# Optimization experiments

Hardware: AMD Instinct MI355X
Metric: run time of the kernel (lower is better)

The kernel has to match this reference:

```python
import jax, jax.numpy as jnp
import numpy as np

NQ = 7
DIM = 2 ** NQ  # 128
N_LAYERS = 3

# Pauli-Z sign tables over the 128 basis states (wire 0 = most significant bit)
_bits = ((np.arange(DIM)[None, :] >> (NQ - 1 - np.arange(NQ)[:, None])) & 1)
_SZ = (1.0 - 2.0 * _bits).astype(np.float32)            # [7, 128]
_SZZ = (_SZ * np.roll(_SZ, -1, axis=0)).astype(np.float32)  # [7, 128], Z_i Z_{(i+1)%7}


def _cnot_perm(c, t):
    # CNOT is a basis-state permutation: flip target bit where control bit = 1
    k = np.arange(DIM)
    return k ^ (((k >> (NQ - 1 - c)) & 1) << (NQ - 1 - t))


def _apply_ry(state, theta, q):
    # state: [B, 128] complex64; theta: [B] or scalar (real)
    B = state.shape[0]
    s = state.reshape(B, 2 ** q, 2, 2 ** (NQ - 1 - q))
    c = jnp.reshape(jnp.cos(0.5 * theta), (-1, 1, 1))
    sn = jnp.reshape(jnp.sin(0.5 * theta), (-1, 1, 1))
    a0, a1 = s[:, :, 0, :], s[:, :, 1, :]
    return jnp.stack([c * a0 - sn * a1, sn * a0 + c * a1], axis=2).reshape(B, DIM)


def _apply_rz(state, theta, q):
    B = state.shape[0]
    s = state.reshape(B, 2 ** q, 2, 2 ** (NQ - 1 - q))
    p = jnp.reshape(jnp.exp(-0.5j * theta), (-1, 1, 1))  # diag(e^{-i t/2}, e^{+i t/2})
    return jnp.stack([p * s[:, :, 0, :], jnp.conj(p) * s[:, :, 1, :]], axis=2).reshape(B, DIM)


def _circuit(x_q, scales, biases, wry, wrz):
    # Batched 7-qubit state-vector simulation of quantum_circuit_v3
    B = x_q.shape[0]
    state = jnp.zeros((B, DIM), jnp.complex64).at[:, 0].set(1.0)
    ang = scales[None, :] * x_q + biases[None, :]  # [B, 7] encoding angles (same every layer)
    for layer in range(N_LAYERS):
        for i in range(NQ):
            state = _apply_ry(state, ang[:, i], i)
        for i in range(NQ):
            state = _apply_ry(state, wry[layer, i], i)
            state = _apply_rz(state, wrz[layer, i], i)
        shift = layer + 1
        for i in range(NQ):
            state = state[:, _cnot_perm(i, (i + shift) % NQ)]
    probs = state.real ** 2 + state.imag ** 2  # [B, 128]
    return jnp.concatenate([probs @ _SZ.T, probs @ _SZZ.T], axis=1)  # [B, 14]


def setup_inputs() -> dict:
    key = jax.random.key(0)
    ks = jax.random.split(key, 16)
    B, F = 32768, 64
    fus_in = 14 + 32 + F  # 110
    lin = lambda k, fi, fo: (0.05 * jax.random.normal(k, (fi, fo), jnp.float32))
    d = {
        "x_q": jax.random.uniform(ks[0], (B, NQ), jnp.float32),
        "x_c": jax.random.normal(ks[1], (B, F), jnp.float32),
        "input_scales": jnp.full((NQ,), np.pi, jnp.float32),
        "input_biases": jnp.zeros((NQ,), jnp.float32),
        "q_params_ry": 0.1 * jax.random.normal(ks[2], (N_LAYERS, NQ), jnp.float32),
        "q_params_rz": 0.1 * jax.random.normal(ks[3], (N_LAYERS, NQ), jnp.float32),
        "enc_w1": lin(ks[4], F, 64), "enc_b1": jnp.zeros((64,), jnp.float32),
        "enc_w2": lin(ks[5], 64, 32), "enc_b2": jnp.zeros((32,), jnp.float32),
        "fus_w1": lin(ks[6], fus_in, 128), "fus_b1": jnp.zeros((128,), jnp.float32),
        "fus_w2": lin(ks[7], 128, 64), "fus_b2": jnp.zeros((64,), jnp.float32),
        "fus_w3": lin(ks[8], 64, 32), "fus_b3": jnp.zeros((32,), jnp.float32),
        "fus_w4": lin(ks[9], 32, 1), "fus_b4": jnp.zeros((1,), jnp.float32),
    }
    return d


def reference(x_q, x_c, input_scales, input_biases, q_params_ry, q_params_rz,
              enc_w1, enc_b1, enc_w2, enc_b2,
              fus_w1, fus_b1, fus_w2, fus_b2, fus_w3, fus_b3, fus_w4, fus_b4):
    q_out = _circuit(x_q, input_scales, input_biases, q_params_ry, q_params_rz)  # [B, 14]
    h = jax.nn.relu(x_c @ enc_w1 + enc_b1)
    c_enc = jax.nn.relu(h @ enc_w2 + enc_b2)  # [B, 32]
    comb = jnp.concatenate([q_out, c_enc, x_c], axis=1)  # [B, 110]
    h = jax.nn.relu(comb @ fus_w1 + fus_b1)
    h = jax.nn.relu(h @ fus_w2 + fus_b2)
    h = jax.nn.relu(h @ fus_w3 + fus_b3)
    return (h @ fus_w4 + fus_b4)[:, 0]  # [B], dropout is identity at inference
```

## Files before the change

kernel.cpp:

```cpp
#include <hip/hip_runtime.h>
#include <math.h>

#define NQ 7
#define DIM 128
#define NLAYERS 3
#define ROWS 64
#define LDS_S 136

typedef __attribute__((ext_vector_type(8))) short bf16x8;
typedef __attribute__((ext_vector_type(4))) float f32x4;
typedef __attribute__((ext_vector_type(2))) float f32x2;
typedef __attribute__((ext_vector_type(4))) unsigned short us4;

__device__ __forceinline__ unsigned short f2bf(float x) {
    union { float f; unsigned int u; } v; v.f = x;
    unsigned int r = v.u + 0x7fff + ((v.u >> 16) & 1);
    return (unsigned short)(r >> 16);
}
__device__ __forceinline__ f32x2 sp(float x) { return (f32x2){x, x}; }
__device__ __forceinline__ f32x2 sel2(int c, f32x2 a, f32x2 b) {
    f32x2 r; r.x = c ? a.x : b.x; r.y = c ? a.y : b.y; return r;
}

constexpr int cperm(int k, int c, int t) {
    return k ^ (((k >> (6 - c)) & 1) << (6 - t));
}
constexpr int lgather(int k, int s) {
    int r = k;
    for (int i = 6; i >= 0; --i) r = cperm(r, i, (i + s) % 7);
    return r;
}

struct Mat { int c[7]; };

constexpr Mat ID{{1, 2, 4, 8, 16, 32, 64}};

constexpr int parity7(int x) { x ^= x >> 4; x ^= x >> 2; x ^= x >> 1; return x & 1; }

constexpr int mapv(const Mat& A, int v) {
    int r = 0;
    for (int j = 0; j < 7; ++j) if ((v >> j) & 1) r ^= A.c[j];
    return r;
}
constexpr Mat matmul(const Mat& A, const Mat& B) {
    Mat m{};
    for (int j = 0; j < 7; ++j) m.c[j] = mapv(A, B.c[j]);
    return m;
}
constexpr Mat matG(int L) {
    Mat m{};
    for (int j = 0; j < 7; ++j) m.c[j] = lgather(1 << j, L + 1);
    return m;
}
constexpr Mat matinv(const Mat& A) {
    int M[7] = {};
    for (int r = 0; r < 7; ++r) {
        int row = 0;
        for (int j = 0; j < 7; ++j) row |= ((A.c[j] >> r) & 1) << j;
        M[r] = row | (1 << (7 + r));
    }
    for (int col = 0; col < 7; ++col) {
        int piv = col;
        while (!((M[piv] >> col) & 1)) ++piv;
        int t = M[col]; M[col] = M[piv]; M[piv] = t;
        for (int r = 0; r < 7; ++r)
            if (r != col && ((M[r] >> col) & 1)) M[r] ^= M[col];
    }
    Mat inv{};
    for (int j = 0; j < 7; ++j) {
        int c = 0;
        for (int r = 0; r < 7; ++r) c |= ((M[r] >> (7 + j)) & 1) << r;
        inv.c[j] = c;
    }
    return inv;
}
constexpr bool isident(const Mat& A) {
    for (int j = 0; j < 7; ++j) if (A.c[j] != (1 << j)) return false;
    return true;
}

constexpr Mat LAM1  = matinv(matG(0));
constexpr Mat LAM2  = matmul(matinv(matG(1)), LAM1);
constexpr Mat LAM3  = matmul(matinv(matG(2)), LAM2);
constexpr Mat LAM1I = matG(0);
constexpr Mat LAM2I = matinv(LAM2);
static_assert(isident(matmul(LAM1, LAM1I)), "lam1 inv");
static_assert(isident(matmul(LAM2, LAM2I)), "lam2 inv");
static_assert(isident(matmul(matG(2), matmul(LAM3, matinv(LAM2)))), "lam3 chain");

constexpr int rowmask(const Mat& A, int b) {
    int r = 0;
    for (int j = 0; j < 7; ++j) r |= ((A.c[j] >> b) & 1) << j;
    return r;
}
constexpr int featM(const Mat& A, int m) {
    int M = 0;
    for (int j = 0; j < 7; ++j) M |= parity7(A.c[j] & m) << j;
    return M;
}
constexpr int szzmask(int i) { return (1 << (6 - i)) | (1 << (6 - ((i + 1) % 7))); }
constexpr int kmask(int k) { return (k < 7) ? (64 >> k) : szzmask(k - 7); }
constexpr unsigned pack_feat(int base) {
    unsigned r = 0;
    for (int j = 0; j < 4; ++j) {
        int k = base + j;
        unsigned e = (k < 14) ? (unsigned)featM(LAM3, kmask(k)) : 0u;
        r |= e << (8 * j);
    }
    return r;
}

template<int M>
__device__ __forceinline__ float xsh(float v) {
    if constexpr (M == 1 || M == 2 || M == 3) {
        constexpr int ctrl = (0 ^ M) | ((1 ^ M) << 2) | ((2 ^ M) << 4) | ((3 ^ M) << 6);
        return __int_as_float(__builtin_amdgcn_update_dpp(
            __float_as_int(v), __float_as_int(v), ctrl, 0xF, 0xF, true));
    } else if constexpr (M == 7) {
        return __int_as_float(__builtin_amdgcn_update_dpp(
            __float_as_int(v), __float_as_int(v), 0x141, 0xF, 0xF, true));
    } else if constexpr (M == 8) {
        return __int_as_float(__builtin_amdgcn_update_dpp(
            __float_as_int(v), __float_as_int(v), 0x128, 0xF, 0xF, true));
    } else if constexpr (M == 15) {
        return __int_as_float(__builtin_amdgcn_update_dpp(
            __float_as_int(v), __float_as_int(v), 0x140, 0xF, 0xF, true));
    } else if constexpr (M < 32) {
        return __int_as_float(__builtin_amdgcn_ds_swizzle(
            __float_as_int(v), (M << 10) | 0x1F));
    } else {
        return __shfl_xor(v, M, 64);
    }
}
template<int M>
__device__ __forceinline__ f32x2 xsh2(f32x2 v) {
    f32x2 r; r.x = xsh<M>(v.x); r.y = xsh<M>(v.y); return r;
}

__device__ __forceinline__ float bpermf(int addr, float v) {
    return __int_as_float(__builtin_amdgcn_ds_bpermute(addr, __float_as_int(v)));
}

template<int D, int R>
__device__ __forceinline__ void ryg(f32x2 c, f32x2 s, int lane,
                                    f32x2& x0r, f32x2& x0i, f32x2& x1r, f32x2& x1i)
{
    constexpr int  DL = D & 63;
    constexpr int  RL = R & 63;
    constexpr bool D6 = (D >> 6) & 1;
    constexpr bool R6 = (R >> 6) & 1;
    int par = __popc(lane & RL) & 1;
    f32x2 ns  = -s;
    f32x2 sg0 = sel2(par, s, ns);
    f32x2 sg1 = R6 ? sel2(par, ns, s) : sg0;
    f32x2 p0r, p0i, p1r, p1i;
    if constexpr (D6) {
        if constexpr (DL == 0) { p0r = x1r; p0i = x1i; p1r = x0r; p1i = x0i; }
        else {
            p0r = xsh2<DL>(x1r); p0i = xsh2<DL>(x1i);
            p1r = xsh2<DL>(x0r); p1i = xsh2<DL>(x0i);
        }
    } else {
        p0r = xsh2<DL>(x0r); p0i = xsh2<DL>(x0i);
        p1r = xsh2<DL>(x1r); p1i = xsh2<DL>(x1i);
    }
    x0r = c * x0r + sg0 * p0r;  x0i = c * x0i + sg0 * p0i;
    x1r = c * x1r + sg1 * p1r;  x1i = c * x1i + sg1 * p1i;
}

template<int LYR, int I>
__device__ __forceinline__ void rygates(
    const float* trig, const f32x2 (&dc)[NQ], const f32x2 (&dsn)[NQ], int lane,
    f32x2& A0r, f32x2& A0i, f32x2& A1r, f32x2& A1i)
{
    if constexpr (I < NQ) {
        constexpr Mat LM  = (LYR == 1) ? LAM1 : LAM2;
        constexpr Mat LMI = (LYR == 1) ? LAM1I : LAM2I;
        constexpr int b   = 6 - I;
        constexpr int D   = mapv(LMI, 1 << b);
        constexpr int R   = rowmask(LM, b);
        float cw = trig[(LYR * NQ + I) * 2 + 0];
        float sw = trig[(LYR * NQ + I) * 2 + 1];
        f32x2 c = dc[I] * sp(cw) - dsn[I] * sp(sw);
        f32x2 s = dsn[I] * sp(cw) + dc[I] * sp(sw);
        ryg<D, R>(c, s, lane, A0r, A0i, A1r, A1i);
        rygates<LYR, I + 1>(trig, dc, dsn, lane, A0r, A0i, A1r, A1i);
    }
}

template<int LYR, int Q>
__device__ __forceinline__ void rzrows(const float* __restrict__ wrz, int lane,
                                       float& Aacc, float& Bacc)
{
    if constexpr (Q < NQ) {
        constexpr Mat LM = (LYR == 0) ? ID : ((LYR == 1) ? LAM1 : LAM2);
        constexpr int R  = rowmask(LM, 6 - Q);
        float h = 0.5f * wrz[LYR * NQ + Q];
        float t = (__popc(lane & (R & 63)) & 1) ? -h : h;
        if constexpr ((R >> 6) & 1) Bacc += t; else Aacc += t;
        rzrows<LYR, Q + 1>(wrz, lane, Aacc, Bacc);
    }
}

template<int LYR>
__device__ __forceinline__ void rzlayer(const float* __restrict__ wrz, int lane,
    f32x2& A0r, f32x2& A0i, f32x2& A1r, f32x2& A1i)
{
    float Aacc = 0.0f, Bacc = 0.0f;
    rzrows<LYR, 0>(wrz, lane, Aacc, Bacc);
    float th0 = Aacc + Bacc, th1 = Aacc - Bacc;
    float c0 = __cosf(th0), s0 = __sinf(th0);
    float c1 = __cosf(th1), s1 = __sinf(th1);
    f32x2 r, im;
    r = A0r; im = A0i;
    A0r = sp(c0) * r  + sp(s0) * im;
    A0i = sp(c0) * im - sp(s0) * r;
    r = A1r; im = A1i;
    A1r = sp(c1) * r  + sp(s1) * im;
    A1i = sp(c1) * im - sp(s1) * r;
}

template<int M>
__device__ __forceinline__ void bfly2(int lane, f32x2& tp, f32x2& tm) {
    f32x2 pp = xsh2<M>(tp), pm = xsh2<M>(tm);
    int hi = lane & M;
    tp = sel2(hi, pp - tp, tp + pp);
    tm = sel2(hi, pm - tm, tm + pm);
}

__global__ __launch_bounds__(256) void circuit_kernel(
    const float* __restrict__ x_q, const float* __restrict__ scales,
    const float* __restrict__ biases,
    const float* __restrict__ wry, const float* __restrict__ wrz,
    const float* __restrict__ ew1, const float* __restrict__ ew2,
    const float* __restrict__ w1,  const float* __restrict__ w2,
    const float* __restrict__ w3,  const float* __restrict__ w4,
    float* __restrict__ q_out,
    unsigned short* __restrict__ ew1t, unsigned short* __restrict__ ew2t,
    unsigned short* __restrict__ w1t,  unsigned short* __restrict__ w2t,
    unsigned short* __restrict__ w3t,  unsigned short* __restrict__ w4t,
    int B)
{
    __shared__ float strig[NLAYERS * NQ * 2];
    const int tid  = threadIdx.x;
    const int lane = tid & 63;

    if (tid < NLAYERS * NQ) {
        float hy = 0.5f * wry[tid];
        strig[tid * 2 + 0] = __cosf(hy);
        strig[tid * 2 + 1] = __sinf(hy);
    }

    if (blockIdx.x < 64) {
        const int gbase  = blockIdx.x * 256 + tid;
        const int stride = 64 * 256;
        for (int i = gbase; i < 16384; i += stride) {
            int n = i >> 7, kp = i & 127;
            unsigned short v = 0;
            if (kp < 64)        v = f2bf(w1[(46 + kp) * 128 + n]);
            else if (kp < 78)   v = f2bf(w1[(kp - 64) * 128 + n]);
            else if (kp < 110)  v = f2bf(w1[(kp - 78 + 14) * 128 + n]);
            w1t[i] = v;
        }
        for (int i = gbase; i < 8192; i += stride) {
            int n = i >> 7, k = i & 127;
            w2t[i] = f2bf(w2[k * 64 + n]);
        }
        for (int i = gbase; i < 4096; i += stride) {
            int n = i >> 6, k = i & 63;
            ew1t[i] = f2bf(ew1[k * 64 + n]);
        }
        for (int i = gbase; i < 2048; i += stride) {
            int n = i >> 6, k = i & 63;
            ew2t[i] = f2bf(ew2[k * 32 + n]);
        }
        for (int i = gbase; i < 2048; i += stride) {
            int n = i >> 6, k = i & 63;
            w3t[i] = f2bf(w3[k * 32 + n]);
        }
        for (int i = gbase; i < 512; i += stride) {
            int n = i >> 5, k = i & 31;
            w4t[i] = (n == 0) ? f2bf(w4[k]) : (unsigned short)0;
        }
    }
    __syncthreads();

    int gtid = blockIdx.x * blockDim.x + tid;
    int wv   = gtid >> 6;
    int e0   = wv * 2;
    if (e0 >= B) return;

    f32x2 dc[NQ], dsn[NQ];
#pragma unroll
    for (int i = 0; i < NQ; ++i) {
        float h0 = 0.5f * fmaf(scales[i], x_q[(size_t)e0 * NQ + i], biases[i]);
        float h1 = 0.5f * fmaf(scales[i], x_q[(size_t)(e0 + 1) * NQ + i], biases[i]);
        dc[i]  = (f32x2){__cosf(h0), __cosf(h1)};
        dsn[i] = (f32x2){__sinf(h0), __sinf(h1)};
    }

    f32x2 A0r, A0i = sp(0.0f), A1r, A1i = sp(0.0f);
    {
        f32x2 cl[NQ], sl[NQ];
#pragma unroll
        for (int i = 0; i < NQ; ++i) {
            float cw = strig[i * 2 + 0], sw = strig[i * 2 + 1];
            cl[i] = dc[i] * sp(cw) - dsn[i] * sp(sw);
            sl[i] = dsn[i] * sp(cw) + dc[i] * sp(sw);
        }
        f32x2 f1 = sel2(lane & 32, sl[1], cl[1]);
        f32x2 f2 = sel2(lane & 16, sl[2], cl[2]);
        f32x2 f3 = sel2(lane &  8, sl[3], cl[3]);
        f32x2 f4 = sel2(lane &  4, sl[4], cl[4]);
        f32x2 f5 = sel2(lane &  2, sl[5], cl[5]);
        f32x2 f6 = sel2(lane &  1, sl[6], cl[6]);
        f32x2 pr = (f1 * f2) * (f3 * f4) * (f5 * f6);
        A0r = pr * cl[0];
        A1r = pr * sl[0];
    }

    rzlayer<0>(wrz, lane, A0r, A0i, A1r, A1i);
    rygates<1, 0>(strig, dc, dsn, lane, A0r, A0i, A1r, A1i);
    rzlayer<1>(wrz, lane, A0r, A0i, A1r, A1i);
    rygates<2, 0>(strig, dc, dsn, lane, A0r, A0i, A1r, A1i);
    rzlayer<2>(wrz, lane, A0r, A0i, A1r, A1i);

    f32x2 p0 = A0r * A0r + A0i * A0i;
    f32x2 p1 = A1r * A1r + A1i * A1i;
    f32x2 tp = p0 + p1;
    f32x2 tm = p0 - p1;

    bfly2<1>(lane, tp, tm);
    bfly2<2>(lane, tp, tm);
    bfly2<4>(lane, tp, tm);
    bfly2<8>(lane, tp, tm);
    bfly2<16>(lane, tp, tm);
    bfly2<32>(lane, tp, tm);

    {
        constexpr unsigned P0 = pack_feat(0),  P1 = pack_feat(4);
        constexpr unsigned P2 = pack_feat(8),  P3 = pack_feat(12);
        int k = lane & 15;
        unsigned wlo  = (k & 4) ? P1 : P0;
        unsigned whi  = (k & 4) ? P3 : P2;
        unsigned word = (k & 8) ? whi : wlo;
        unsigned entry = (word >> ((k & 3) * 8)) & 127u;
        int addr   = (int)(entry & 63u) << 2;
        int useTm  = (int)(entry & 64u);
        int e      = (lane >> 4) & 1;
        float vpx = bpermf(addr, tp.x), vpy = bpermf(addr, tp.y);
        float vmx = bpermf(addr, tm.x), vmy = bpermf(addr, tm.y);
        float vp = e ? vpy : vpx;
        float vm = e ? vmy : vmx;
        float val = useTm ? vm : vp;
        if (lane < 32) q_out[(size_t)e0 * 16 + lane] = val;
    }
}

template<int K, int NT, bool RELU>
__device__ __forceinline__ void wlayer(
    const unsigned short* src, unsigned short* dst,
    const unsigned short* __restrict__ wt, const float* __restrict__ bias,
    int dstcol, int lane)
{
    constexpr int KB = K / 32;
    const int lcol = lane & 15;
    const int lrow = lane >> 4;

    bf16x8 a[KB];
#pragma unroll
    for (int kb = 0; kb < KB; ++kb)
        a[kb] = *(const bf16x8*)&src[lcol * LDS_S + kb * 32 + lrow * 8];

#pragma unroll
    for (int n = 0; n < NT; ++n) {
        float bb = bias[n * 16 + lcol];
        f32x4 acc = (f32x4){bb, bb, bb, bb};
#pragma unroll
        for (int kb = 0; kb < KB; ++kb) {
            bf16x8 b = *(const bf16x8*)&wt[(n * 16 + lcol) * K + kb * 32 + lrow * 8];
            acc = __builtin_amdgcn_mfma_f32_16x16x32_bf16(a[kb], b, acc, 0, 0, 0);
        }
#pragma unroll
        for (int r = 0; r < 4; ++r) {
            float v = acc[r];
            if (RELU) v = fmaxf(v, 0.0f);
            dst[(lrow * 4 + r) * LDS_S + dstcol + n * 16 + lcol] = f2bf(v);
        }
    }
}

__global__ __launch_bounds__(256) void mlp_kernel(
    const float* __restrict__ q_out, const float* __restrict__ x_c,
    const unsigned short* __restrict__ ew1t, const float* __restrict__ eb1,
    const unsigned short* __restrict__ ew2t, const float* __restrict__ eb2,
    const unsigned short* __restrict__ w1t,  const float* __restrict__ b1,
    const unsigned short* __restrict__ w2t,  const float* __restrict__ b2,
    const unsigned short* __restrict__ w3t,  const float* __restrict__ b3,
    const unsigned short* __restrict__ w4t,  const float* __restrict__ b4,
    float* __restrict__ out, int B)
{
    __shared__ unsigned short Buf[4 * 2 * 16 * LDS_S];

    const int tid   = threadIdx.x;
    const int lane  = tid & 63;
    const int wv    = tid >> 6;
    const int rbase = blockIdx.x * ROWS + wv * 16;

    unsigned short* bufA = Buf + wv * (2 * 16 * LDS_S);
    unsigned short* bufB = bufA + 16 * LDS_S;

    {
        const int srow = lane >> 2;
#pragma unroll
        for (int it = 0; it < 4; ++it) {
            int fc = (lane & 3) + it * 4;
            float4 v = *(const float4*)&x_c[(size_t)(rbase + srow) * 64 + fc * 4];
            us4 b;
            b.x = f2bf(v.x); b.y = f2bf(v.y); b.z = f2bf(v.z); b.w = f2bf(v.w);
            *(us4*)&bufA[srow * LDS_S + fc * 4] = b;
        }
    }
#pragma unroll
    for (int it = 0; it < 4; ++it) {
        int idx = lane + it * 64;
        int row = idx >> 4, k = idx & 15;
        bufA[row * LDS_S + 64 + k] = f2bf(q_out[(size_t)(rbase + row) * 16 + k]);
    }
#pragma unroll
    for (int it = 0; it < 2; ++it) {
        int idx = lane + it * 64;
        int row = idx >> 3, j = idx & 7;
        *(unsigned int*)&bufA[row * LDS_S + 112 + 2 * j] = 0;
    }
    if (lane < 16) *(unsigned int*)&bufA[lane * LDS_S + 110] = 0;

    wlayer< 64, 4, true>(bufA, bufB, ew1t, eb1,  0, lane);
    wlayer< 64, 2, true>(bufB, bufA, ew2t, eb2, 78, lane);
    wlayer<128, 8, true>(bufA, bufB, w1t,  b1,   0, lane);
    wlayer<128, 4, true>(bufB, bufA, w2t,  b2,   0, lane);
    wlayer< 64, 2, true>(bufA, bufB, w3t,  b3,   0, lane);

    {
        const int lcol = lane & 15;
        const int lrow = lane >> 4;
        bf16x8 a = *(const bf16x8*)&bufB[lcol * LDS_S + lrow * 8];
        bf16x8 b = *(const bf16x8*)&w4t[lcol * 32 + lrow * 8];
        float bv = b4[0];
        f32x4 acc = (f32x4){bv, bv, bv, bv};
        acc = __builtin_amdgcn_mfma_f32_16x16x32_bf16(a, b, acc, 0, 0, 0);
        if (lcol == 0) {
            float4 o; o.x = acc[0]; o.y = acc[1]; o.z = acc[2]; o.w = acc[3];
            *(float4*)(out + rbase + lrow * 4) = o;
        }
    }
}

extern "C" void kernel_launch(void* const* d_in, const int* in_sizes, int n_in,
                              void* d_out, int out_size, void* d_ws, size_t ws_size,
                              hipStream_t stream)
{
    const float* x_q     = (const float*)d_in[0];
    const float* x_c     = (const float*)d_in[1];
    const float* scales  = (const float*)d_in[2];
    const float* biases  = (const float*)d_in[3];
    const float* wry     = (const float*)d_in[4];
    const float* wrz     = (const float*)d_in[5];
    const float* enc_w1  = (const float*)d_in[6];
    const float* enc_b1  = (const float*)d_in[7];
    const float* enc_w2  = (const float*)d_in[8];
    const float* enc_b2  = (const float*)d_in[9];
    const float* fus_w1  = (const float*)d_in[10];
    const float* fus_b1  = (const float*)d_in[11];
    const float* fus_w2  = (const float*)d_in[12];
    const float* fus_b2  = (const float*)d_in[13];
    const float* fus_w3  = (const float*)d_in[14];
    const float* fus_b3  = (const float*)d_in[15];
    const float* fus_w4  = (const float*)d_in[16];
    const float* fus_b4  = (const float*)d_in[17];
    float* out = (float*)d_out;

    int B = in_sizes[0] / NQ;

    float* ws    = (float*)d_ws;
    float* q_out = ws;
    unsigned short* wsh = (unsigned short*)(q_out + (size_t)B * 16);
    unsigned short* w1t  = wsh;
    unsigned short* w2t  = w1t + 16384;
    unsigned short* ew1t = w2t + 8192;
    unsigned short* ew2t = ew1t + 4096;
    unsigned short* w3t  = ew2t + 2048;
    unsigned short* w4t  = w3t + 2048;

    int circ_blocks = ((B / 2) * 64 + 255) / 256;
    circuit_kernel<<<circ_blocks, 256, 0, stream>>>(
        x_q, scales, biases, wry, wrz,
        enc_w1, enc_w2, fus_w1, fus_w2, fus_w3, fus_w4,
        q_out, ew1t, ew2t, w1t, w2t, w3t, w4t, B);

    int row_blocks = B / ROWS;
    mlp_kernel<<<row_blocks, 256, 0, stream>>>(q_out, x_c,
                                               ew1t, enc_b1, ew2t, enc_b2,
                                               w1t, fus_b1, w2t, fus_b2,
                                               w3t, fus_b3, w4t, fus_b4,
                                               out, B);
}
```

Before: 41.93 us.

## Share MLP activations across block waves and split output tiles per wave

The MLP kernel previously had each wave process its own 16 rows independently and load every weight tile for all outputs. Now the 64-row block shares LDS activation buffers, and each wave owns a subset of output column tiles (or row tiles when tiles are few). The waves keep their weight fragments in registers and reuse them across row tiles, with __syncthreads between layers. The aim is to cut redundant global weight reads per wave, at the cost of block-wide barriers. Launch bounds also now request 4 blocks per CU.

```diff
diff --git a/kernel.cpp b/kernel.cpp
--- a/kernel.cpp
+++ b/kernel.cpp
@@ -357,40 +357,58 @@
     }
 }
 
-template<int K, int NT, bool RELU>
-__device__ __forceinline__ void wlayer(
+template<int K, int NTILES, bool RELU>
+__device__ __forceinline__ void layer_mfma(
     const unsigned short* src, unsigned short* dst,
     const unsigned short* __restrict__ wt, const float* __restrict__ bias,
-    int dstcol, int lane)
-{
-    constexpr int KB = K / 32;
+    int dstcol, int lane, int wv)
+{
+    constexpr int KB   = K / 32;
+    constexpr int NT_W = (NTILES > 4) ? NTILES / 4 : 1;
+    constexpr int MT_W = NTILES / NT_W;
+    const int ntile0 = (wv * NT_W) % NTILES;
+    const int mtile0 = ((wv * NT_W) / NTILES) * MT_W;
     const int lcol = lane & 15;
     const int lrow = lane >> 4;
 
-    bf16x8 a[KB];
-#pragma unroll
-    for (int kb = 0; kb < KB; ++kb)
-        a[kb] = *(const bf16x8*)&src[lcol * LDS_S + kb * 32 + lrow * 8];
-
-#pragma unroll
-    for (int n = 0; n < NT; ++n) {
-        float bb = bias[n * 16 + lcol];
-        f32x4 acc = (f32x4){bb, bb, bb, bb};
-#pragma unroll
-        for (int kb = 0; kb < KB; ++kb) {
-            bf16x8 b = *(const bf16x8*)&wt[(n * 16 + lcol) * K + kb * 32 + lrow * 8];
-            acc = __builtin_amdgcn_mfma_f32_16x16x32_bf16(a[kb], b, acc, 0, 0, 0);
-        }
-#pragma unroll
-        for (int r = 0; r < 4; ++r) {
-            float v = acc[r];
-            if (RELU) v = fmaxf(v, 0.0f);
-            dst[(lrow * 4 + r) * LDS_S + dstcol + n * 16 + lcol] = f2bf(v);
-        }
-    }
-}
-
-__global__ __launch_bounds__(256) void mlp_kernel(
+    bf16x8 bfrag[NT_W][KB];
+    float  bb[NT_W];
+#pragma unroll
+    for (int n = 0; n < NT_W; ++n) {
+#pragma unroll
+        for (int kb = 0; kb < KB; ++kb)
+            bfrag[n][kb] = *(const bf16x8*)&wt[((ntile0 + n) * 16 + lcol) * K + kb * 32 + lrow * 8];
+        bb[n] = bias[(ntile0 + n) * 16 + lcol];
+    }
+
+#pragma unroll
+    for (int m = 0; m < MT_W; ++m) {
+        bf16x8 afrag[KB];
+#pragma unroll
+        for (int kb = 0; kb < KB; ++kb)
+            afrag[kb] = *(const bf16x8*)&src[((mtile0 + m) * 16 + lcol) * LDS_S + kb * 32 + lrow * 8];
+
+        f32x4 acc[NT_W];
+#pragma unroll
+        for (int n = 0; n < NT_W; ++n) acc[n] = (f32x4){bb[n], bb[n], bb[n], bb[n]};
+#pragma unroll
+        for (int kb = 0; kb < KB; ++kb)
+#pragma unroll
+            for (int n = 0; n < NT_W; ++n)
+                acc[n] = __builtin_amdgcn_mfma_f32_16x16x32_bf16(afrag[kb], bfrag[n][kb], acc[n], 0, 0, 0);
+
+#pragma unroll
+        for (int n = 0; n < NT_W; ++n)
+#pragma unroll
+            for (int r = 0; r < 4; ++r) {
+                float v = acc[n][r];
+                if (RELU) v = fmaxf(v, 0.0f);
+                dst[((mtile0 + m) * 16 + lrow * 4 + r) * LDS_S + dstcol + (ntile0 + n) * 16 + lcol] = f2bf(v);
+            }
+    }
+}
+
+__global__ __launch_bounds__(256, 4) void mlp_kernel(
     const float* __restrict__ q_out, const float* __restrict__ x_c,
     const unsigned short* __restrict__ ew1t, const float* __restrict__ eb1,
     const unsigned short* __restrict__ ew2t, const float* __restrict__ eb2,
@@ -400,58 +418,56 @@
     const unsigned short* __restrict__ w4t,  const float* __restrict__ b4,
     float* __restrict__ out, int B)
 {
-    __shared__ unsigned short Buf[4 * 2 * 16 * LDS_S];
-
-    const int tid   = threadIdx.x;
-    const int lane  = tid & 63;
-    const int wv    = tid >> 6;
-    const int rbase = blockIdx.x * ROWS + wv * 16;
-
-    unsigned short* bufA = Buf + wv * (2 * 16 * LDS_S);
-    unsigned short* bufB = bufA + 16 * LDS_S;
+    __shared__ unsigned short BufA[ROWS * LDS_S];
+    __shared__ unsigned short BufB[ROWS * LDS_S];
+
+    const int tid  = threadIdx.x;
+    const int lane = tid & 63;
+    const int wv   = __builtin_amdgcn_readfirstlane(tid >> 6);
+    const int base = blockIdx.x * ROWS;
 
     {
-        const int srow = lane >> 2;
-#pragma unroll
-        for (int it = 0; it < 4; ++it) {
-            int fc = (lane & 3) + it * 4;
-            float4 v = *(const float4*)&x_c[(size_t)(rbase + srow) * 64 + fc * 4];
+        const float4* xr = (const float4*)(x_c + (size_t)base * 64);
+        for (int i = tid; i < 1024; i += 256) {
+            int row = i >> 4, fc = i & 15;
+            float4 v = xr[i];
             us4 b;
             b.x = f2bf(v.x); b.y = f2bf(v.y); b.z = f2bf(v.z); b.w = f2bf(v.w);
-            *(us4*)&bufA[srow * LDS_S + fc * 4] = b;
-        }
-    }
-#pragma unroll
-    for (int it = 0; it < 4; ++it) {
-        int idx = lane + it * 64;
-        int row = idx >> 4, k = idx & 15;
-        bufA[row * LDS_S + 64 + k] = f2bf(q_out[(size_t)(rbase + row) * 16 + k]);
-    }
-#pragma unroll
-    for (int it = 0; it < 2; ++it) {
-        int idx = lane + it * 64;
-        int row = idx >> 3, j = idx & 7;
-        *(unsigned int*)&bufA[row * LDS_S + 112 + 2 * j] = 0;
-    }
-    if (lane < 16) *(unsigned int*)&bufA[lane * LDS_S + 110] = 0;
-
-    wlayer< 64, 4, true>(bufA, bufB, ew1t, eb1,  0, lane);
-    wlayer< 64, 2, true>(bufB, bufA, ew2t, eb2, 78, lane);
-    wlayer<128, 8, true>(bufA, bufB, w1t,  b1,   0, lane);
-    wlayer<128, 4, true>(bufB, bufA, w2t,  b2,   0, lane);
-    wlayer< 64, 2, true>(bufA, bufB, w3t,  b3,   0, lane);
+            *(us4*)&BufA[row * LDS_S + fc * 4] = b;
+        }
+    }
+    for (int i = tid; i < 1024; i += 256) {
+        int row = i >> 4, k = i & 15;
+        BufA[row * LDS_S + 64 + k] = f2bf(q_out[(size_t)(base + row) * 16 + k]);
+    }
+    for (int i = tid; i < 64 * 18; i += 256) {
+        int row = i / 18, k = i - row * 18;
+        BufA[row * LDS_S + 110 + k] = 0;
+    }
+    __syncthreads();
+
+    layer_mfma<64, 4, true>(BufA, BufB, ew1t, eb1, 0, lane, wv);
+    __syncthreads();
+    layer_mfma<64, 2, true>(BufB, BufA, ew2t, eb2, 78, lane, wv);
+    __syncthreads();
+    layer_mfma<128, 8, true>(BufA, BufB, w1t, b1, 0, lane, wv);
+    __syncthreads();
+    layer_mfma<128, 4, true>(BufB, BufA, w2t, b2, 0, lane, wv);
+    __syncthreads();
+    layer_mfma<64, 2, true>(BufA, BufB, w3t, b3, 0, lane, wv);
+    __syncthreads();
 
     {
         const int lcol = lane & 15;
         const int lrow = lane >> 4;
-        bf16x8 a = *(const bf16x8*)&bufB[lcol * LDS_S + lrow * 8];
+        bf16x8 a = *(const bf16x8*)&BufB[(wv * 16 + lcol) * LDS_S + lrow * 8];
         bf16x8 b = *(const bf16x8*)&w4t[lcol * 32 + lrow * 8];
         float bv = b4[0];
         f32x4 acc = (f32x4){bv, bv, bv, bv};
         acc = __builtin_amdgcn_mfma_f32_16x16x32_bf16(a, b, acc, 0, 0, 0);
         if (lcol == 0) {
             float4 o; o.x = acc[0]; o.y = acc[1]; o.z = acc[2]; o.w = acc[3];
-            *(float4*)(out + rbase + lrow * 4) = o;
+            *(float4*)(out + base + wv * 16 + lrow * 4) = o;
         }
     }
 }
```

After: 34.91 us. 1.2x faster.
